# Kernel optimization log

Hardware: AMD Instinct MI355X
Metric: run time of the kernel (lower is better)

The kernel has to match this reference:

```python
import jax, jax.numpy as jnp
import numpy as np

B, S, HID = 2, 2048, 5120
H = 32
D_NOPE, D_ROPE, D_V = 128, 64, 128
D_Q = D_NOPE + D_ROPE          # 192, q/k head dim
Q_RANK, KV_RANK = 1536, 512
THETA = 10000.0
EPS = 1e-6


def setup_inputs() -> dict:
    key = jax.random.key(0)
    ks = jax.random.split(key, 8)
    w = lambda k, shape: jax.random.normal(k, shape, jnp.float32) * 0.02
    hidden_states = jax.random.normal(ks[0], (B, S, HID), jnp.float32)
    position_ids = jnp.broadcast_to(jnp.arange(S, dtype=jnp.int32), (B, S))
    attention_mask = jnp.broadcast_to(
        jnp.tril(jnp.ones((S, S), bool))[None, None], (B, 1, S, S))
    return {
        "hidden_states": hidden_states,
        "q_a_proj_w": w(ks[1], (Q_RANK, HID)),
        "q_a_ln_w": jnp.ones((Q_RANK,), jnp.float32),
        "q_b_proj_w": w(ks[2], (H * D_Q, Q_RANK)),
        "kv_a_proj_w": w(ks[3], (KV_RANK + D_ROPE, HID)),
        "kv_a_ln_w": jnp.ones((KV_RANK,), jnp.float32),
        "kv_b_proj_w": w(ks[4], (H * (D_NOPE + D_V), KV_RANK)),
        "o_proj_w": w(ks[5], (HID, H * D_V)),
        "position_ids": position_ids,
        "attention_mask": attention_mask,
    }


def _rms_norm(x, w, eps=EPS):
    x32 = x.astype(jnp.float32)
    var = jnp.mean(x32 * x32, axis=-1, keepdims=True)
    return (x32 * jax.lax.rsqrt(var + eps)).astype(x.dtype) * w


def _deinterleave(x):
    # view(..., d//2, 2).transpose(-1, -2).reshape(..., d)
    return jnp.concatenate([x[..., 0::2], x[..., 1::2]], axis=-1)


def _rotate_half(x):
    h = x.shape[-1] // 2
    return jnp.concatenate([-x[..., h:], x[..., :h]], axis=-1)


def _mla_forward(hidden_states, q_a_proj_w, q_a_ln_w, q_b_proj_w,
                 kv_a_proj_w, kv_a_ln_w, kv_b_proj_w, o_proj_w,
                 position_ids, attention_mask):
    b, s, _ = hidden_states.shape
    # low-rank Q path
    q_c = hidden_states @ q_a_proj_w.T                        # [b,s,Q_RANK]
    q = _rms_norm(q_c, q_a_ln_w) @ q_b_proj_w.T               # [b,s,H*D_Q]
    q = q.reshape(b, s, H, D_Q).transpose(0, 2, 1, 3)         # [b,H,s,D_Q]
    q_nope, q_pe = q[..., :D_NOPE], q[..., D_NOPE:]
    # compressed KV path (MQA rope part shared across heads)
    ckv = hidden_states @ kv_a_proj_w.T                       # [b,s,KV_RANK+D_ROPE]
    compressed, k_pe = ckv[..., :KV_RANK], ckv[..., KV_RANK:]
    k_pe = k_pe.reshape(b, s, 1, D_ROPE).transpose(0, 2, 1, 3)  # [b,1,s,D_ROPE]
    kv = _rms_norm(compressed, kv_a_ln_w) @ kv_b_proj_w.T     # [b,s,H*(D_NOPE+D_V)]
    kv = kv.reshape(b, s, H, D_NOPE + D_V).transpose(0, 2, 1, 3)
    k_nope, v = kv[..., :D_NOPE], kv[..., D_NOPE:]
    # decoupled RoPE (interleaved layout, DeepSeek-V2 style)
    inv_freq = 1.0 / (THETA ** (jnp.arange(0, D_ROPE, 2, dtype=jnp.float32) / D_ROPE))
    t = jnp.arange(s, dtype=jnp.float32)
    emb = jnp.concatenate([t[:, None] * inv_freq, t[:, None] * inv_freq], axis=-1)
    cos = jnp.cos(emb)[position_ids][:, None]                 # [b,1,s,D_ROPE]
    sin = jnp.sin(emb)[position_ids][:, None]
    q_pe = _deinterleave(q_pe)
    k_pe = _deinterleave(k_pe)
    q_pe = q_pe * cos + _rotate_half(q_pe) * sin
    k_pe = k_pe * cos + _rotate_half(k_pe) * sin
    # assemble full q/k and attend
    query = jnp.concatenate([q_nope, q_pe], axis=-1)          # [b,H,s,D_Q]
    key = jnp.concatenate(
        [k_nope, jnp.broadcast_to(k_pe, (b, H, s, D_ROPE))], axis=-1)
    scale = D_Q ** -0.5
    scores = jnp.einsum('bhqd,bhkd->bhqk', query, key) * scale
    scores = jnp.where(attention_mask, scores, jnp.float32(-1e9))
    probs = jax.nn.softmax(scores.astype(jnp.float32), axis=-1).astype(query.dtype)
    attn = jnp.einsum('bhqk,bhkd->bhqd', probs, v)            # [b,H,s,D_V]
    attn = attn.transpose(0, 2, 1, 3).reshape(b, s, H * D_V)
    return attn @ o_proj_w.T                                   # [b,s,HID]


def reference(hidden_states, q_a_proj_w, q_a_ln_w, q_b_proj_w,
              kv_a_proj_w, kv_a_ln_w, kv_b_proj_w, o_proj_w,
              position_ids, attention_mask):
    return _mla_forward(hidden_states, q_a_proj_w, q_a_ln_w, q_b_proj_w,
                        kv_a_proj_w, kv_a_ln_w, kv_b_proj_w, o_proj_w,
                        position_ids, attention_mask)
```

## Files before the change

kernel.cpp:

```cpp
#include <hip/hip_runtime.h>
#include <hip/hip_bf16.h>

typedef __bf16 bf16_t;
typedef __bf16 bf16x4 __attribute__((ext_vector_type(4)));
typedef __bf16 bf16x8 __attribute__((ext_vector_type(8)));
typedef float f32x4 __attribute__((ext_vector_type(4)));

#define B_ 2
#define S_ 2048
#define HID_ 5120
#define H_ 32
#define D_NOPE_ 128
#define D_ROPE_ 64
#define D_V_ 128
#define D_Q_ 192
#define EPS_ 1e-6f

#define GLDS16(g, l)                                                          \
  __builtin_amdgcn_global_load_lds(                                           \
      (const __attribute__((address_space(1))) void*)(g),                     \
      (__attribute__((address_space(3))) void*)(l), 16, 0, 0)

__global__ __launch_bounds__(256) void f32_to_bf16_k(const float* __restrict__ x,
                                                     bf16_t* __restrict__ y, long n) {
  long i = ((long)blockIdx.x * 256 + threadIdx.x) * 8;
  if (i + 8 <= n) {
    float4 f0 = *(const float4*)(x + i);
    float4 f1 = *(const float4*)(x + i + 4);
    bf16x8 o;
    o[0] = (bf16_t)f0.x; o[1] = (bf16_t)f0.y; o[2] = (bf16_t)f0.z; o[3] = (bf16_t)f0.w;
    o[4] = (bf16_t)f1.x; o[5] = (bf16_t)f1.y; o[6] = (bf16_t)f1.z; o[7] = (bf16_t)f1.w;
    *(bf16x8*)(y + i) = o;
  }
}

template <int CMODE>
__global__ __launch_bounds__(256) void gemm128(const bf16_t* __restrict__ A,
                                               const bf16_t* __restrict__ W,
                                               void* __restrict__ Cv,
                                               bf16_t* __restrict__ vTp,
                                               int M, int N, int K) {
  __shared__ bf16_t As[128 * 32];
  __shared__ bf16_t Ws[128 * 32];
  const int tid = threadIdx.x;
  const int lane = tid & 63;
  const int wave = tid >> 6;
  const int bm = blockIdx.y * 128;
  const int bn = blockIdx.x * 128;
  const int wm = (wave >> 1) * 64;
  const int wn = (wave & 1) * 64;
  const int ll = lane & 15;
  const int kg = (lane >> 4) * 8;
  const int r0 = tid >> 2;
  const int cc0 = (tid & 3) * 8;
  const bf16_t* Ag0 = A + (size_t)(bm + r0) * K + cc0;
  const bf16_t* Ag1 = A + (size_t)(bm + 64 + r0) * K + cc0;
  const bf16_t* Wg0 = W + (size_t)(bn + r0) * K + cc0;
  const bf16_t* Wg1 = W + (size_t)(bn + 64 + r0) * K + cc0;
  bf16_t* Al0 = &As[tid * 8];
  bf16_t* Al1 = &As[(tid + 256) * 8];
  bf16_t* Wl0 = &Ws[tid * 8];
  bf16_t* Wl1 = &Ws[(tid + 256) * 8];

  f32x4 acc[4][4];
#pragma unroll
  for (int m = 0; m < 4; m++)
#pragma unroll
    for (int n = 0; n < 4; n++) acc[m][n] = {};

  for (int k0 = 0; k0 < K; k0 += 32) {
    GLDS16(Ag0 + k0, Al0);
    GLDS16(Ag1 + k0, Al1);
    GLDS16(Wg0 + k0, Wl0);
    GLDS16(Wg1 + k0, Wl1);
    __syncthreads();
    bf16x8 af[4], bfr[4];
#pragma unroll
    for (int m = 0; m < 4; m++)
      af[m] = *(const bf16x8*)&As[(wm + m * 16 + ll) * 32 + kg];
#pragma unroll
    for (int n = 0; n < 4; n++)
      bfr[n] = *(const bf16x8*)&Ws[(wn + n * 16 + ll) * 32 + kg];
#pragma unroll
    for (int m = 0; m < 4; m++)
#pragma unroll
      for (int n = 0; n < 4; n++)
        acc[m][n] = __builtin_amdgcn_mfma_f32_16x16x32_bf16(af[m], bfr[n], acc[m][n], 0, 0, 0);
    __syncthreads();
  }

  const int rb = (lane >> 4) * 4;
  if constexpr (CMODE == 2) {
    bf16_t* KN = (bf16_t*)Cv;
#pragma unroll
    for (int m = 0; m < 4; m++)
#pragma unroll
      for (int n = 0; n < 4; n++) {
        int mrow = bm + wm + m * 16 + rb;
        int nn = bn + wn + n * 16 + ll;
        int hh = nn >> 8, cc = nn & 255;
        if (cc < 128) {
          bf16_t* p = KN + ((size_t)mrow * H_ + hh) * 128 + cc;
#pragma unroll
          for (int rr = 0; rr < 4; rr++)
            p[(size_t)rr * (H_ * 128)] = (bf16_t)acc[m][n][rr];
        } else {
          int bb = mrow >> 11;
          int s0 = mrow & 2047;
          bf16x4 o;
          o[0] = (bf16_t)acc[m][n][0]; o[1] = (bf16_t)acc[m][n][1];
          o[2] = (bf16_t)acc[m][n][2]; o[3] = (bf16_t)acc[m][n][3];
          *(bf16x4*)(vTp + (((size_t)bb * H_ + hh) * 128 + (cc - 128)) * S_ + s0) = o;
        }
      }
  } else {
#pragma unroll
    for (int m = 0; m < 4; m++)
#pragma unroll
      for (int n = 0; n < 4; n++) {
        int row = bm + wm + m * 16 + rb;
        int col = bn + wn + n * 16 + ll;
        if (CMODE == 1) {
          float* C = (float*)Cv;
#pragma unroll
          for (int rr = 0; rr < 4; rr++)
            C[(size_t)(row + rr) * N + col] = acc[m][n][rr];
        } else {
          bf16_t* C = (bf16_t*)Cv;
#pragma unroll
          for (int rr = 0; rr < 4; rr++)
            C[(size_t)(row + rr) * N + col] = (bf16_t)acc[m][n][rr];
        }
      }
  }
}

__global__ __launch_bounds__(256) void gemm_bt64(const bf16_t* __restrict__ A,
                                                 const bf16_t* __restrict__ W,
                                                 bf16_t* __restrict__ C,
                                                 int M, int N, int K) {
  __shared__ bf16_t As[64 * 40];
  __shared__ bf16_t Ws[64 * 40];
  const int tid = threadIdx.x;
  const int bm = blockIdx.y * 64;
  const int bn = blockIdx.x * 64;
  const int wave = tid >> 6, lane = tid & 63;
  const int wm = (wave >> 1) * 32, wn = (wave & 1) * 32;
  const int srow = tid >> 2;
  const int scol = (tid & 3) * 8;
  const bf16_t* Ap16 = A + (size_t)(bm + srow) * K + scol;
  const bf16_t* Wp = W + (size_t)(bn + srow) * K + scol;
  f32x4 acc00 = {}, acc01 = {}, acc10 = {}, acc11 = {};
  const int r = lane & 15;
  const int kq = (lane >> 4) * 8;
  for (int k0 = 0; k0 < K; k0 += 32) {
    *(bf16x8*)&As[srow * 40 + scol] = *(const bf16x8*)(Ap16 + k0);
    *(bf16x8*)&Ws[srow * 40 + scol] = *(const bf16x8*)(Wp + k0);
    __syncthreads();
    bf16x8 a0 = *(bf16x8*)&As[(wm + r) * 40 + kq];
    bf16x8 a1 = *(bf16x8*)&As[(wm + 16 + r) * 40 + kq];
    bf16x8 b0 = *(bf16x8*)&Ws[(wn + r) * 40 + kq];
    bf16x8 b1 = *(bf16x8*)&Ws[(wn + 16 + r) * 40 + kq];
    acc00 = __builtin_amdgcn_mfma_f32_16x16x32_bf16(a0, b0, acc00, 0, 0, 0);
    acc01 = __builtin_amdgcn_mfma_f32_16x16x32_bf16(a0, b1, acc01, 0, 0, 0);
    acc10 = __builtin_amdgcn_mfma_f32_16x16x32_bf16(a1, b0, acc10, 0, 0, 0);
    acc11 = __builtin_amdgcn_mfma_f32_16x16x32_bf16(a1, b1, acc11, 0, 0, 0);
    __syncthreads();
  }
  const int col = lane & 15;
  const int rb = (lane >> 4) * 4;
#pragma unroll
  for (int rr = 0; rr < 4; rr++) {
    int m0r = bm + wm + rb + rr;
    int m1r = m0r + 16;
    C[(size_t)m0r * N + (bn + wn + col)]      = (bf16_t)acc00[rr];
    C[(size_t)m0r * N + (bn + wn + 16 + col)] = (bf16_t)acc01[rr];
    C[(size_t)m1r * N + (bn + wn + col)]      = (bf16_t)acc10[rr];
    C[(size_t)m1r * N + (bn + wn + 16 + col)] = (bf16_t)acc11[rr];
  }
}

__global__ __launch_bounds__(256) void rmsnorm_k(const bf16_t* __restrict__ x,
                                                 const float* __restrict__ w,
                                                 bf16_t* __restrict__ y,
                                                 int dim, int xstride) {
  const int row = blockIdx.x;
  const bf16_t* xr = x + (size_t)row * xstride;
  bf16_t* yr = y + (size_t)row * dim;
  float ss = 0.f;
  for (int i = threadIdx.x; i < dim; i += 256) {
    float v = (float)xr[i];
    ss += v * v;
  }
  for (int off = 32; off > 0; off >>= 1) ss += __shfl_down(ss, off);
  __shared__ float red[4];
  __shared__ float s_rinv;
  if ((threadIdx.x & 63) == 0) red[threadIdx.x >> 6] = ss;
  __syncthreads();
  if (threadIdx.x == 0) {
    float tot = red[0] + red[1] + red[2] + red[3];
    s_rinv = 1.0f / sqrtf(tot / (float)dim + EPS_);
  }
  __syncthreads();
  float rinv = s_rinv;
  for (int i = threadIdx.x; i < dim; i += 256)
    yr[i] = (bf16_t)((float)xr[i] * rinv * w[i]);
}

__global__ __launch_bounds__(64) void rope_k(const bf16_t* __restrict__ src,
                                             bf16_t* __restrict__ dst,
                                             const int* __restrict__ pos_ids,
                                             int heads_per_pos, int sstride,
                                             int dstride) {
  __shared__ float xs[64];
  const int rrow = blockIdx.x;
  const int j = threadIdx.x;
  const bf16_t* s = src + (size_t)rrow * sstride;
  xs[j] = (float)s[j];
  __syncthreads();
  const int pos = pos_ids[rrow / heads_per_pos];
  const int i = j & 31;
  float freq = exp2f(-(float)i * 0.4152410118609203f);
  float ang = (float)pos * freq;
  float c, sn;
  __sincosf(ang, &sn, &c);
  float outv;
  if (j < 32)
    outv = xs[2 * j] * c - xs[2 * j + 1] * sn;
  else
    outv = xs[2 * i + 1] * c + xs[2 * i] * sn;
  dst[(size_t)rrow * dstride + j] = (bf16_t)outv;
}

__global__ __launch_bounds__(512, 4) void flash_attn3(
    const bf16_t* __restrict__ q, const bf16_t* __restrict__ knope,
    const bf16_t* __restrict__ kpe, const bf16_t* __restrict__ vT,
    bf16_t* __restrict__ attn) {
  __shared__ bf16_t KF[12288];
  __shared__ bf16_t VF[8192];
  __shared__ bf16_t PF[8192];
  const int tid = threadIdx.x;
  const int w = tid >> 6;
  const int lane = tid & 63;
  const int ll = lane & 15;
  const int g0 = lane >> 4;
  const int bh = blockIdx.y;
  const int b = bh >> 5;
  const int h = bh & 31;
  const int q0 = ((int)gridDim.x - 1 - (int)blockIdx.x) * 128;
  const int bS = b * S_;
  bf16_t* PFw = PF + w * 1024;

  const float qsc = 0.07216878364870322f * 1.4426950408889634f;
  bf16x8 qf[6];
#pragma unroll
  for (int ks = 0; ks < 6; ks++) {
    bf16x8 raw = *(const bf16x8*)(
        q + (((size_t)(bS + q0 + 16 * w + ll)) * H_ + h) * D_Q_ + 32 * ks + 8 * g0);
    bf16x8 sc;
#pragma unroll
    for (int j = 0; j < 8; j++) sc[j] = (bf16_t)((float)raw[j] * qsc);
    qf[ks] = sc;
  }

  f32x4 acc[8];
#pragma unroll
  for (int dt = 0; dt < 8; dt++) acc[dt] = {};
  float m_run = -1e30f, l_run = 0.f;

  const bf16_t* kptr[3];
  int kstr[3];
#pragma unroll
  for (int i = 0; i < 3; i++) {
    int c = tid + 512 * i;
    int t_ = c / 384;
    int rem = c - t_ * 384;
    int ks_ = rem >> 6;
    int g_ = (rem >> 4) & 3;
    int ll_ = c & 15;
    int row = 16 * t_ + ll_;
    int k = 32 * ks_ + 8 * g_;
    if (k < 128) {
      kptr[i] = knope + ((size_t)(bS + row) * H_ + h) * 128 + k;
      kstr[i] = H_ * 128;
    } else {
      kptr[i] = kpe + (size_t)(bS + row) * 64 + (k - 128);
      kstr[i] = 64;
    }
  }
  const bf16_t* vptr[2];
#pragma unroll
  for (int i = 0; i < 2; i++) {
    int c = tid + 512 * i;
    int ll_ = c & 15;
    int g_ = (c >> 4) & 3;
    int ks2_ = (c >> 6) & 1;
    int dt_ = c >> 7;
    vptr[i] = vT + (((size_t)b * H_ + h) * 128 + 16 * dt_ + ll_) * S_ +
              32 * ks2_ + 8 * g_;
  }

  bf16x8 kst[3], vst[2];
  auto load_kv = [&]() {
#pragma unroll
    for (int i = 0; i < 3; i++) kst[i] = *(const bf16x8*)kptr[i];
#pragma unroll
    for (int i = 0; i < 2; i++) vst[i] = *(const bf16x8*)vptr[i];
#pragma unroll
    for (int i = 0; i < 3; i++) kptr[i] += (size_t)64 * kstr[i];
#pragma unroll
    for (int i = 0; i < 2; i++) vptr[i] += 64;
  };

  load_kv();
  const int nkt = (q0 >> 6) + 2;

  for (int kt = 0; kt < nkt; kt++) {
    const int k0 = kt * 64;
    __syncthreads();
#pragma unroll
    for (int i = 0; i < 3; i++) *(bf16x8*)&KF[(tid + 512 * i) * 8] = kst[i];
#pragma unroll
    for (int i = 0; i < 2; i++) *(bf16x8*)&VF[(tid + 512 * i) * 8] = vst[i];
    __syncthreads();
    if (kt + 1 < nkt) load_kv();

    f32x4 sv[4];
#pragma unroll
    for (int t = 0; t < 4; t++) sv[t] = {};
    __builtin_amdgcn_s_setprio(1);
#pragma unroll
    for (int ks = 0; ks < 6; ks++) {
      bf16x8 bq = qf[ks];
#pragma unroll
      for (int t = 0; t < 4; t++) {
        bf16x8 ak = *(bf16x8*)&KF[(t * 6 + ks) * 512 + lane * 8];
        sv[t] = __builtin_amdgcn_mfma_f32_16x16x32_bf16(ak, bq, sv[t], 0, 0, 0);
      }
    }
    __builtin_amdgcn_s_setprio(0);

    const int qg = q0 + 16 * w + ll;
    float mx = m_run;
    if (k0 + 63 > q0 + 16 * w) {
#pragma unroll
      for (int t = 0; t < 4; t++)
#pragma unroll
        for (int r = 0; r < 4; r++) {
          float s = sv[t][r];
          s = (k0 + 16 * t + 4 * g0 + r > qg) ? -1e30f : s;
          sv[t][r] = s;
          mx = fmaxf(mx, s);
        }
    } else {
#pragma unroll
      for (int t = 0; t < 4; t++)
#pragma unroll
        for (int r = 0; r < 4; r++) mx = fmaxf(mx, sv[t][r]);
    }
    mx = fmaxf(mx, __shfl_xor(mx, 16));
    mx = fmaxf(mx, __shfl_xor(mx, 32));
    float al = exp2f(m_run - mx);
    float rs = 0.f;
#pragma unroll
    for (int t = 0; t < 4; t++) {
      bf16x4 pv;
#pragma unroll
      for (int r = 0; r < 4; r++) {
        float p = exp2f(sv[t][r] - mx);
        rs += p;
        pv[r] = (bf16_t)p;
      }
      int elem = ((t >> 1) * 4 + 2 * (t & 1) + (g0 >> 1)) * 128 + ll * 8 + 4 * (g0 & 1);
      *(bf16x4*)&PFw[elem] = pv;
    }
    rs += __shfl_xor(rs, 16);
    rs += __shfl_xor(rs, 32);
    l_run = l_run * al + rs;
    m_run = mx;

#pragma unroll
    for (int r = 0; r < 4; r++) {
      float a = __shfl(al, 4 * g0 + r);
#pragma unroll
      for (int dt = 0; dt < 8; dt++) acc[dt][r] *= a;
    }

    __builtin_amdgcn_s_setprio(1);
#pragma unroll
    for (int ks2 = 0; ks2 < 2; ks2++) {
      bf16x8 ap = *(bf16x8*)&PFw[ks2 * 512 + lane * 8];
#pragma unroll
      for (int dt = 0; dt < 8; dt++) {
        bf16x8 bv = *(bf16x8*)&VF[(dt * 2 + ks2) * 512 + lane * 8];
        acc[dt] = __builtin_amdgcn_mfma_f32_16x16x32_bf16(ap, bv, acc[dt], 0, 0, 0);
      }
    }
    __builtin_amdgcn_s_setprio(0);
  }

  float linv = 1.f / l_run;
#pragma unroll
  for (int r = 0; r < 4; r++) {
    float inv = __shfl(linv, 4 * g0 + r);
    int qrow = q0 + 16 * w + 4 * g0 + r;
    bf16_t* op = attn + (((size_t)(bS + qrow)) * H_ + h) * D_V_ + ll;
#pragma unroll
    for (int dt = 0; dt < 8; dt++)
      op[dt * 16] = (bf16_t)(acc[dt][r] * inv);
  }
}

extern "C" void kernel_launch(void* const* d_in, const int* in_sizes, int n_in,
                              void* d_out, int out_size, void* d_ws, size_t ws_size,
                              hipStream_t stream) {
  const float* hidden  = (const float*)d_in[0];
  const float* q_a_w   = (const float*)d_in[1];
  const float* q_a_ln  = (const float*)d_in[2];
  const float* q_b_w   = (const float*)d_in[3];
  const float* kv_a_w  = (const float*)d_in[4];
  const float* kv_a_ln = (const float*)d_in[5];
  const float* kv_b_w  = (const float*)d_in[6];
  const float* o_w     = (const float*)d_in[7];
  const int*   pos_ids = (const int*)d_in[8];
  float* out = (float*)d_out;
  char* ws = (char*)d_ws;
  const int M = B_ * S_;

  bf16_t* q_ws   = (bf16_t*)(ws + 0);
  bf16_t* knope_ws=(bf16_t*)(ws + 50331648);
  bf16_t* vT_ws  = (bf16_t*)(ws + 83886080);
  bf16_t* kpe_ws = (bf16_t*)(ws + 117440512);
  bf16_t* Wslot  = (bf16_t*)(ws + 117964800);
  bf16_t* qc_ws  = (bf16_t*)(ws + 159907840);
  bf16_t* qcn_ws = (bf16_t*)(ws + 172490752);
  bf16_t* ckv_ws = (bf16_t*)(ws + 185073664);
  bf16_t* ckvn_ws= (bf16_t*)(ws + 189792256);
  bf16_t* attn_ws= (bf16_t*)(ws + 159907840);
  bf16_t* hid_bf = (bf16_t*)(ws + 50331648);

  f32_to_bf16_k<<<(int)((4096L * 5120) / 2048), 256, 0, stream>>>(hidden, hid_bf, 4096L * 5120);
  f32_to_bf16_k<<<1536 * 5120 / 2048, 256, 0, stream>>>(q_a_w, Wslot, 1536L * 5120);
  gemm128<0><<<dim3(1536 / 128, M / 128), 256, 0, stream>>>(hid_bf, Wslot, qc_ws, nullptr, M, 1536, 5120);
  rmsnorm_k<<<M, 256, 0, stream>>>(qc_ws, q_a_ln, qcn_ws, 1536, 1536);
  f32_to_bf16_k<<<576 * 5120 / 2048, 256, 0, stream>>>(kv_a_w, Wslot, 576L * 5120);
  gemm_bt64<<<dim3(576 / 64, M / 64), 256, 0, stream>>>(hid_bf, Wslot, ckv_ws, M, 576, 5120);
  rmsnorm_k<<<M, 256, 0, stream>>>(ckv_ws, kv_a_ln, ckvn_ws, 512, 576);
  f32_to_bf16_k<<<6144 * 1536 / 2048, 256, 0, stream>>>(q_b_w, Wslot, 6144L * 1536);
  gemm128<0><<<dim3(6144 / 128, M / 128), 256, 0, stream>>>(qcn_ws, Wslot, q_ws, nullptr, M, 6144, 1536);
  f32_to_bf16_k<<<8192 * 512 / 2048, 256, 0, stream>>>(kv_b_w, Wslot, 8192L * 512);
  gemm128<2><<<dim3(8192 / 128, M / 128), 256, 0, stream>>>(ckvn_ws, Wslot, knope_ws, vT_ws, M, 8192, 512);
  rope_k<<<M * H_, 64, 0, stream>>>(q_ws + 128, q_ws + 128, pos_ids, H_, D_Q_, D_Q_);
  rope_k<<<M, 64, 0, stream>>>(ckv_ws + 512, kpe_ws, pos_ids, 1, 576, 64);
  flash_attn3<<<dim3(S_ / 128, B_ * H_), 512, 0, stream>>>(q_ws, knope_ws, kpe_ws, vT_ws, attn_ws);
  f32_to_bf16_k<<<5120 * 4096 / 2048, 256, 0, stream>>>(o_w, Wslot, 5120L * 4096);
  gemm128<1><<<dim3(5120 / 128, M / 128), 256, 0, stream>>>(attn_ws, Wslot, out, nullptr, M, 5120, 4096);
}
```

Baseline: 1.239 ms.

## Pre-tile K/V into MFMA fragment layout and switch attention to 32x32 MFMA

```diff
diff --git a/kernel.cpp b/kernel.cpp
--- a/kernel.cpp
+++ b/kernel.cpp
@@ -5,6 +5,7 @@
 typedef __bf16 bf16x4 __attribute__((ext_vector_type(4)));
 typedef __bf16 bf16x8 __attribute__((ext_vector_type(8)));
 typedef float f32x4 __attribute__((ext_vector_type(4)));
+typedef float f32x16 __attribute__((ext_vector_type(16)));
 
 #define B_ 2
 #define S_ 2048
@@ -98,19 +99,23 @@
       for (int n = 0; n < 4; n++) {
         int mrow = bm + wm + m * 16 + rb;
         int nn = bn + wn + n * 16 + ll;
-        int hh = nn >> 8, cc = nn & 255;
+        int hh2 = nn >> 8, cc = nn & 255;
+        int bb = mrow >> 11, s = mrow & 2047;
+        size_t tile = (size_t)(bb * H_ + hh2) * 32 + (s >> 6);
         if (cc < 128) {
-          bf16_t* p = KN + ((size_t)mrow * H_ + hh) * 128 + cc;
-#pragma unroll
-          for (int rr = 0; rr < 4; rr++)
-            p[(size_t)rr * (H_ * 128)] = (bf16_t)acc[m][n][rr];
+          int t = (s >> 5) & 1, ml = s & 31, kc = cc >> 4, hb = (cc >> 3) & 1, j = cc & 7;
+          bf16_t* p = KN + tile * 8192 + (size_t)(((t * 8 + kc) * 64 + 32 * hb + ml) * 8 + j);
+#pragma unroll
+          for (int rr = 0; rr < 4; rr++) p[rr * 8] = (bf16_t)acc[m][n][rr];
         } else {
-          int bb = mrow >> 11;
-          int s0 = mrow & 2047;
+          int d = cc - 128;
+          int kc2 = (s >> 4) & 3, hb = (s >> 3) & 1, jb = s & 7;
+          int dn = d >> 5, dl = d & 31;
           bf16x4 o;
           o[0] = (bf16_t)acc[m][n][0]; o[1] = (bf16_t)acc[m][n][1];
           o[2] = (bf16_t)acc[m][n][2]; o[3] = (bf16_t)acc[m][n][3];
-          *(bf16x4*)(vTp + (((size_t)bb * H_ + hh) * 128 + (cc - 128)) * S_ + s0) = o;
+          *(bf16x4*)(vTp + tile * 8192 +
+                     (size_t)(((dn * 4 + kc2) * 64 + 32 * hb + dl) * 8 + jb)) = o;
         }
       }
   } else {
@@ -232,182 +237,189 @@
   dst[(size_t)rrow * dstride + j] = (bf16_t)outv;
 }
 
-__global__ __launch_bounds__(512, 4) void flash_attn3(
-    const bf16_t* __restrict__ q, const bf16_t* __restrict__ knope,
-    const bf16_t* __restrict__ kpe, const bf16_t* __restrict__ vT,
+__global__ __launch_bounds__(64) void rope_kpe_k(const bf16_t* __restrict__ src,
+                                                 bf16_t* __restrict__ kpeF,
+                                                 const int* __restrict__ pos_ids) {
+  __shared__ float xs[64];
+  const int rrow = blockIdx.x;
+  const int j = threadIdx.x;
+  const bf16_t* s = src + (size_t)rrow * 576;
+  xs[j] = (float)s[j];
+  __syncthreads();
+  const int pos = pos_ids[rrow];
+  const int i = j & 31;
+  float freq = exp2f(-(float)i * 0.4152410118609203f);
+  float ang = (float)pos * freq;
+  float c, sn;
+  __sincosf(ang, &sn, &c);
+  float outv = (j < 32) ? xs[2 * j] * c - xs[2 * j + 1] * sn
+                        : xs[2 * i + 1] * c + xs[2 * i] * sn;
+  int bb = rrow >> 11, ss = rrow & 2047;
+  int t64 = ss >> 6, t = (ss >> 5) & 1, ml = ss & 31;
+  kpeF[(size_t)(bb * 32 + t64) * 4096 +
+       (size_t)(((t * 4 + (j >> 4)) * 64 + 32 * ((j >> 3) & 1) + ml) * 8 + (j & 7))] =
+      (bf16_t)outv;
+}
+
+__global__ __launch_bounds__(256) void flash_attn4(
+    const bf16_t* __restrict__ q, const bf16_t* __restrict__ knF,
+    const bf16_t* __restrict__ kpeF, const bf16_t* __restrict__ vF,
     bf16_t* __restrict__ attn) {
   __shared__ bf16_t KF[12288];
   __shared__ bf16_t VF[8192];
-  __shared__ bf16_t PF[8192];
   const int tid = threadIdx.x;
   const int w = tid >> 6;
   const int lane = tid & 63;
-  const int ll = lane & 15;
-  const int g0 = lane >> 4;
+  const int ql = lane & 31;
+  const int hh = lane >> 5;
   const int bh = blockIdx.y;
-  const int b = bh >> 5;
-  const int h = bh & 31;
+  const int b = bh >> 5, h = bh & 31;
   const int q0 = ((int)gridDim.x - 1 - (int)blockIdx.x) * 128;
   const int bS = b * S_;
-  bf16_t* PFw = PF + w * 1024;
 
   const float qsc = 0.07216878364870322f * 1.4426950408889634f;
-  bf16x8 qf[6];
-#pragma unroll
-  for (int ks = 0; ks < 6; ks++) {
-    bf16x8 raw = *(const bf16x8*)(
-        q + (((size_t)(bS + q0 + 16 * w + ll)) * H_ + h) * D_Q_ + 32 * ks + 8 * g0);
-    bf16x8 sc;
-#pragma unroll
-    for (int j = 0; j < 8; j++) sc[j] = (bf16_t)((float)raw[j] * qsc);
-    qf[ks] = sc;
-  }
-
-  f32x4 acc[8];
-#pragma unroll
-  for (int dt = 0; dt < 8; dt++) acc[dt] = {};
+  bf16x8 qf[12];
+  {
+    const bf16_t* qp = q + (((size_t)(bS + q0 + 32 * w + ql)) * H_ + h) * D_Q_ + 8 * hh;
+#pragma unroll
+    for (int kc = 0; kc < 12; kc++) {
+      bf16x8 raw = *(const bf16x8*)(qp + 16 * kc);
+      bf16x8 sc;
+#pragma unroll
+      for (int j = 0; j < 8; j++) sc[j] = (bf16_t)((float)raw[j] * qsc);
+      qf[kc] = sc;
+    }
+  }
+
+  f32x16 acc0 = {}, acc1 = {}, acc2 = {}, acc3 = {};
   float m_run = -1e30f, l_run = 0.f;
 
-  const bf16_t* kptr[3];
-  int kstr[3];
-#pragma unroll
-  for (int i = 0; i < 3; i++) {
-    int c = tid + 512 * i;
-    int t_ = c / 384;
-    int rem = c - t_ * 384;
-    int ks_ = rem >> 6;
-    int g_ = (rem >> 4) & 3;
-    int ll_ = c & 15;
-    int row = 16 * t_ + ll_;
-    int k = 32 * ks_ + 8 * g_;
-    if (k < 128) {
-      kptr[i] = knope + ((size_t)(bS + row) * H_ + h) * 128 + k;
-      kstr[i] = H_ * 128;
-    } else {
-      kptr[i] = kpe + (size_t)(bS + row) * 64 + (k - 128);
-      kstr[i] = 64;
-    }
-  }
-  const bf16_t* vptr[2];
-#pragma unroll
-  for (int i = 0; i < 2; i++) {
-    int c = tid + 512 * i;
-    int ll_ = c & 15;
-    int g_ = (c >> 4) & 3;
-    int ks2_ = (c >> 6) & 1;
-    int dt_ = c >> 7;
-    vptr[i] = vT + (((size_t)b * H_ + h) * 128 + 16 * dt_ + ll_) * S_ +
-              32 * ks2_ + 8 * g_;
-  }
-
-  bf16x8 kst[3], vst[2];
-  auto load_kv = [&]() {
-#pragma unroll
-    for (int i = 0; i < 3; i++) kst[i] = *(const bf16x8*)kptr[i];
-#pragma unroll
-    for (int i = 0; i < 2; i++) vst[i] = *(const bf16x8*)vptr[i];
-#pragma unroll
-    for (int i = 0; i < 3; i++) kptr[i] += (size_t)64 * kstr[i];
-#pragma unroll
-    for (int i = 0; i < 2; i++) vptr[i] += 64;
-  };
-
-  load_kv();
+  const bf16_t* kn_src = knF + (size_t)(b * H_ + h) * 262144 + (w * 512 + lane * 8);
+  const bf16_t* kp_src = kpeF + (size_t)b * 131072 + (w * 512 + lane * 8);
+  const bf16_t* v_src  = vF + (size_t)(b * H_ + h) * 262144 + tid * 8;
+
   const int nkt = (q0 >> 6) + 2;
+  const int qg = q0 + 32 * w + ql;
 
   for (int kt = 0; kt < nkt; kt++) {
     const int k0 = kt * 64;
-    __syncthreads();
-#pragma unroll
-    for (int i = 0; i < 3; i++) *(bf16x8*)&KF[(tid + 512 * i) * 8] = kst[i];
-#pragma unroll
-    for (int i = 0; i < 2; i++) *(bf16x8*)&VF[(tid + 512 * i) * 8] = vst[i];
-    __syncthreads();
-    if (kt + 1 < nkt) load_kv();
-
-    f32x4 sv[4];
-#pragma unroll
-    for (int t = 0; t < 4; t++) sv[t] = {};
+    GLDS16(kn_src,        &KF[(tid       ) * 8]);
+    GLDS16(kn_src + 2048, &KF[(tid +  256) * 8]);
+    GLDS16(kp_src,        &KF[(tid +  512) * 8]);
+    GLDS16(kn_src + 4096, &KF[(tid +  768) * 8]);
+    GLDS16(kn_src + 6144, &KF[(tid + 1024) * 8]);
+    GLDS16(kp_src + 2048, &KF[(tid + 1280) * 8]);
+    GLDS16(v_src,         &VF[(tid       ) * 8]);
+    GLDS16(v_src + 2048,  &VF[(tid +  256) * 8]);
+    GLDS16(v_src + 4096,  &VF[(tid +  512) * 8]);
+    GLDS16(v_src + 6144,  &VF[(tid +  768) * 8]);
+    kn_src += 8192; kp_src += 4096; v_src += 8192;
+    __syncthreads();
+
+    f32x16 sv0 = {}, sv1 = {};
     __builtin_amdgcn_s_setprio(1);
 #pragma unroll
-    for (int ks = 0; ks < 6; ks++) {
-      bf16x8 bq = qf[ks];
-#pragma unroll
-      for (int t = 0; t < 4; t++) {
-        bf16x8 ak = *(bf16x8*)&KF[(t * 6 + ks) * 512 + lane * 8];
-        sv[t] = __builtin_amdgcn_mfma_f32_16x16x32_bf16(ak, bq, sv[t], 0, 0, 0);
-      }
+    for (int kc = 0; kc < 12; kc++) {
+      bf16x8 ak0 = *(bf16x8*)&KF[(kc * 64 + lane) * 8];
+      bf16x8 ak1 = *(bf16x8*)&KF[((12 + kc) * 64 + lane) * 8];
+      sv0 = __builtin_amdgcn_mfma_f32_32x32x16_bf16(ak0, qf[kc], sv0, 0, 0, 0);
+      sv1 = __builtin_amdgcn_mfma_f32_32x32x16_bf16(ak1, qf[kc], sv1, 0, 0, 0);
     }
     __builtin_amdgcn_s_setprio(0);
 
-    const int qg = q0 + 16 * w + ll;
-    float mx = m_run;
-    if (k0 + 63 > q0 + 16 * w) {
-#pragma unroll
-      for (int t = 0; t < 4; t++)
-#pragma unroll
-        for (int r = 0; r < 4; r++) {
-          float s = sv[t][r];
-          s = (k0 + 16 * t + 4 * g0 + r > qg) ? -1e30f : s;
-          sv[t][r] = s;
-          mx = fmaxf(mx, s);
+    float tmax = -1e30f;
+    if (k0 + 63 > q0 + 32 * w) {
+#pragma unroll
+      for (int r = 0; r < 16; r++) {
+        int kvr = (r & 3) + 8 * (r >> 2) + 4 * hh;
+        float s0 = sv0[r]; if (k0 + kvr > qg) s0 = -1e30f;
+        sv0[r] = s0; tmax = fmaxf(tmax, s0);
+        float s1 = sv1[r]; if (k0 + 32 + kvr > qg) s1 = -1e30f;
+        sv1[r] = s1; tmax = fmaxf(tmax, s1);
+      }
+    } else {
+#pragma unroll
+      for (int r = 0; r < 16; r++) {
+        tmax = fmaxf(tmax, sv0[r]);
+        tmax = fmaxf(tmax, sv1[r]);
+      }
+    }
+    tmax = fmaxf(tmax, __shfl_xor(tmax, 32));
+    bool need = tmax > m_run + 10.0f;
+    float mnew = need ? fmaxf(m_run, tmax) : m_run;
+    float al = exp2f(m_run - mnew);
+    float rs = 0.f;
+#pragma unroll
+    for (int r = 0; r < 16; r++) {
+      float p0 = exp2f(sv0[r] - mnew); sv0[r] = p0; rs += p0;
+      float p1 = exp2f(sv1[r] - mnew); sv1[r] = p1; rs += p1;
+    }
+    rs += __shfl_xor(rs, 32);
+    if (__any(need)) {
+#pragma unroll
+      for (int r = 0; r < 16; r++) {
+        float ar = __shfl(al, (r & 3) + 8 * (r >> 2) + 4 * hh);
+        acc0[r] *= ar; acc1[r] *= ar; acc2[r] *= ar; acc3[r] *= ar;
+      }
+    }
+    l_run = l_run * al + rs;
+    m_run = mnew;
+
+    bf16x8 pa[4];
+#pragma unroll
+    for (int t = 0; t < 2; t++) {
+#pragma unroll
+      for (int qd = 0; qd < 2; qd++) {
+        bf16x4 qe, qo;
+#pragma unroll
+        for (int e = 0; e < 4; e++) {
+          float pe = (t == 0) ? sv0[8 * qd + e]     : sv1[8 * qd + e];
+          float po = (t == 0) ? sv0[8 * qd + 4 + e] : sv1[8 * qd + 4 + e];
+          qe[e] = (bf16_t)pe;
+          qo[e] = (bf16_t)po;
         }
-    } else {
-#pragma unroll
-      for (int t = 0; t < 4; t++)
-#pragma unroll
-        for (int r = 0; r < 4; r++) mx = fmaxf(mx, sv[t][r]);
-    }
-    mx = fmaxf(mx, __shfl_xor(mx, 16));
-    mx = fmaxf(mx, __shfl_xor(mx, 32));
-    float al = exp2f(m_run - mx);
-    float rs = 0.f;
-#pragma unroll
-    for (int t = 0; t < 4; t++) {
-      bf16x4 pv;
-#pragma unroll
-      for (int r = 0; r < 4; r++) {
-        float p = exp2f(sv[t][r] - mx);
-        rs += p;
-        pv[r] = (bf16_t)p;
-      }
-      int elem = ((t >> 1) * 4 + 2 * (t & 1) + (g0 >> 1)) * 128 + ll * 8 + 4 * (g0 & 1);
-      *(bf16x4*)&PFw[elem] = pv;
-    }
-    rs += __shfl_xor(rs, 16);
-    rs += __shfl_xor(rs, 32);
-    l_run = l_run * al + rs;
-    m_run = mx;
-
-#pragma unroll
-    for (int r = 0; r < 4; r++) {
-      float a = __shfl(al, 4 * g0 + r);
-#pragma unroll
-      for (int dt = 0; dt < 8; dt++) acc[dt][r] *= a;
+        bf16x4 kept = hh ? qo : qe;
+        bf16x4 sent = hh ? qe : qo;
+        unsigned long long su = *(unsigned long long*)&sent;
+        unsigned long long ru = __shfl_xor(su, 32);
+        bf16x4 recv = *(bf16x4*)&ru;
+        bf16x8 f;
+#pragma unroll
+        for (int e = 0; e < 4; e++) {
+          f[e]     = hh ? recv[e] : kept[e];
+          f[4 + e] = hh ? kept[e] : recv[e];
+        }
+        pa[2 * t + qd] = f;
+      }
     }
 
     __builtin_amdgcn_s_setprio(1);
 #pragma unroll
-    for (int ks2 = 0; ks2 < 2; ks2++) {
-      bf16x8 ap = *(bf16x8*)&PFw[ks2 * 512 + lane * 8];
-#pragma unroll
-      for (int dt = 0; dt < 8; dt++) {
-        bf16x8 bv = *(bf16x8*)&VF[(dt * 2 + ks2) * 512 + lane * 8];
-        acc[dt] = __builtin_amdgcn_mfma_f32_16x16x32_bf16(ap, bv, acc[dt], 0, 0, 0);
-      }
+    for (int kc2 = 0; kc2 < 4; kc2++) {
+      bf16x8 bv0 = *(bf16x8*)&VF[((0 * 4 + kc2) * 64 + lane) * 8];
+      bf16x8 bv1 = *(bf16x8*)&VF[((1 * 4 + kc2) * 64 + lane) * 8];
+      bf16x8 bv2 = *(bf16x8*)&VF[((2 * 4 + kc2) * 64 + lane) * 8];
+      bf16x8 bv3 = *(bf16x8*)&VF[((3 * 4 + kc2) * 64 + lane) * 8];
+      acc0 = __builtin_amdgcn_mfma_f32_32x32x16_bf16(pa[kc2], bv0, acc0, 0, 0, 0);
+      acc1 = __builtin_amdgcn_mfma_f32_32x32x16_bf16(pa[kc2], bv1, acc1, 0, 0, 0);
+      acc2 = __builtin_amdgcn_mfma_f32_32x32x16_bf16(pa[kc2], bv2, acc2, 0, 0, 0);
+      acc3 = __builtin_amdgcn_mfma_f32_32x32x16_bf16(pa[kc2], bv3, acc3, 0, 0, 0);
     }
     __builtin_amdgcn_s_setprio(0);
+    __syncthreads();
   }
 
   float linv = 1.f / l_run;
 #pragma unroll
-  for (int r = 0; r < 4; r++) {
-    float inv = __shfl(linv, 4 * g0 + r);
-    int qrow = q0 + 16 * w + 4 * g0 + r;
-    bf16_t* op = attn + (((size_t)(bS + qrow)) * H_ + h) * D_V_ + ll;
-#pragma unroll
-    for (int dt = 0; dt < 8; dt++)
-      op[dt * 16] = (bf16_t)(acc[dt][r] * inv);
+  for (int r = 0; r < 16; r++) {
+    int qr = (r & 3) + 8 * (r >> 2) + 4 * hh;
+    float inv = __shfl(linv, qr);
+    int qrow = q0 + 32 * w + qr;
+    bf16_t* op = attn + (((size_t)(bS + qrow)) * H_ + h) * D_V_ + ql;
+    op[0]  = (bf16_t)(acc0[r] * inv);
+    op[32] = (bf16_t)(acc1[r] * inv);
+    op[64] = (bf16_t)(acc2[r] * inv);
+    op[96] = (bf16_t)(acc3[r] * inv);
   }
 }
 
@@ -428,9 +440,9 @@
   const int M = B_ * S_;
 
   bf16_t* q_ws   = (bf16_t*)(ws + 0);
-  bf16_t* knope_ws=(bf16_t*)(ws + 50331648);
-  bf16_t* vT_ws  = (bf16_t*)(ws + 83886080);
-  bf16_t* kpe_ws = (bf16_t*)(ws + 117440512);
+  bf16_t* knF_ws = (bf16_t*)(ws + 50331648);
+  bf16_t* vF_ws  = (bf16_t*)(ws + 83886080);
+  bf16_t* kpeF_ws= (bf16_t*)(ws + 117440512);
   bf16_t* Wslot  = (bf16_t*)(ws + 117964800);
   bf16_t* qc_ws  = (bf16_t*)(ws + 159907840);
   bf16_t* qcn_ws = (bf16_t*)(ws + 172490752);
@@ -449,10 +461,10 @@
   f32_to_bf16_k<<<6144 * 1536 / 2048, 256, 0, stream>>>(q_b_w, Wslot, 6144L * 1536);
   gemm128<0><<<dim3(6144 / 128, M / 128), 256, 0, stream>>>(qcn_ws, Wslot, q_ws, nullptr, M, 6144, 1536);
   f32_to_bf16_k<<<8192 * 512 / 2048, 256, 0, stream>>>(kv_b_w, Wslot, 8192L * 512);
-  gemm128<2><<<dim3(8192 / 128, M / 128), 256, 0, stream>>>(ckvn_ws, Wslot, knope_ws, vT_ws, M, 8192, 512);
+  gemm128<2><<<dim3(8192 / 128, M / 128), 256, 0, stream>>>(ckvn_ws, Wslot, knF_ws, vF_ws, M, 8192, 512);
   rope_k<<<M * H_, 64, 0, stream>>>(q_ws + 128, q_ws + 128, pos_ids, H_, D_Q_, D_Q_);
-  rope_k<<<M, 64, 0, stream>>>(ckv_ws + 512, kpe_ws, pos_ids, 1, 576, 64);
-  flash_attn3<<<dim3(S_ / 128, B_ * H_), 512, 0, stream>>>(q_ws, knope_ws, kpe_ws, vT_ws, attn_ws);
+  rope_kpe_k<<<M, 64, 0, stream>>>(ckv_ws + 512, kpeF_ws, pos_ids);
+  flash_attn4<<<dim3(S_ / 128, B_ * H_), 256, 0, stream>>>(q_ws, knF_ws, kpeF_ws, vF_ws, attn_ws);
   f32_to_bf16_k<<<5120 * 4096 / 2048, 256, 0, stream>>>(o_w, Wslot, 5120L * 4096);
   gemm128<1><<<dim3(5120 / 128, M / 128), 256, 0, stream>>>(attn_ws, Wslot, out, nullptr, M, 5120, 4096);
 }
```

New measurement: 1.277 ms. 1.03x slower.
